# Kernel tuning notes

Hardware: AMD Instinct MI355X
Metric: run time of the kernel (lower is better)

## Reference

```python
import jax, jax.numpy as jnp
import numpy as np
from jax import lax

TEMP = 0.05
MOMENTUM = 0.9
EPS = 1e-12


def _l2_normalize(x, axis=-1):
    n = jnp.sqrt(jnp.sum(x * x, axis=axis, keepdims=True))
    return x / jnp.maximum(n, EPS)


def _cross_entropy(logits, targets):
    # mean over batch of -log_softmax(logits)[target]
    logp = jax.nn.log_softmax(logits, axis=-1)
    return -jnp.mean(jnp.take_along_axis(logp, targets[:, None], axis=-1))


def _momentum_update(features, x, targets, m):
    # Sequential per-sample read-modify-write (faithful to the torch loop,
    # matters when targets contain duplicates). carry = memory bank.
    def step(f, xy):
        x_i, y_i = xy
        row = m * f[y_i] + (1.0 - m) * x_i
        row = row / jnp.linalg.norm(row)
        return f.at[y_i].set(row), None
    f, _ = lax.scan(step, features, (x, targets))
    return f


def setup_inputs() -> dict:
    key = jax.random.key(0)
    k1, k2, k3, k4, k5, k6 = jax.random.split(key, 6)
    B, D, N = 512, 1024, 16384
    inputs_rgb = jax.random.normal(k1, (B, D), dtype=jnp.float32)
    inputs_ir = jax.random.normal(k2, (B, D), dtype=jnp.float32)
    targets_rgb = jax.random.randint(k3, (B,), 0, N, dtype=jnp.int32)
    targets_ir = jax.random.randint(k4, (B,), 0, N, dtype=jnp.int32)
    # memory banks (buffers); initialized as normalized random rows to mimic a
    # warmed-up cluster memory (the module starts at zeros, degenerate for CE)
    features_rgb = _l2_normalize(jax.random.normal(k5, (N, D), dtype=jnp.float32))
    features_ir = _l2_normalize(jax.random.normal(k6, (N, D), dtype=jnp.float32))
    return {"inputs_rgb": inputs_rgb, "inputs_ir": inputs_ir,
            "targets_rgb": targets_rgb, "targets_ir": targets_ir,
            "features_rgb": features_rgb, "features_ir": features_ir}


def reference(inputs_rgb, inputs_ir, targets_rgb, targets_ir, features_rgb, features_ir):
    x_rgb = _l2_normalize(inputs_rgb)  # [B, D]
    x_ir = _l2_normalize(inputs_ir)
    logits_rgb = (x_rgb @ features_rgb.T) / TEMP  # [B, N]
    logits_ir = (x_ir @ features_ir.T) / TEMP
    loss_rgb = _cross_entropy(logits_rgb, targets_rgb)
    loss_ir = _cross_entropy(logits_ir, targets_ir)
    # side-effect of CM.backward in the original: momentum scatter update + renorm
    # (change_scale == 1.0 so the Hungarian cross-modal exchange is skipped)
    new_features_rgb = _momentum_update(features_rgb, x_rgb, targets_rgb, MOMENTUM)
    new_features_ir = _momentum_update(features_ir, x_ir, targets_ir, MOMENTUM)
    return (loss_rgb, loss_ir, new_features_rgb, new_features_ir)
```

## Files before the change

kernel.cpp:

```cpp
#include <hip/hip_runtime.h>
#include <math.h>

#define BATCH 512
#define DIM   1024
#define NCLUS 16384
#define TINV  20.0f

typedef __attribute__((ext_vector_type(4))) float f32x4;
typedef __attribute__((ext_vector_type(8))) short bf16x8;

static __device__ __forceinline__ unsigned short f2bf(float f) {
  unsigned int u = __float_as_uint(f);
  u += 0x7FFFu + ((u >> 16) & 1u);
  return (unsigned short)(u >> 16);
}

typedef const __attribute__((address_space(1))) unsigned int* gas1_t;
typedef __attribute__((address_space(3))) unsigned int* las3_t;
static __device__ __forceinline__ void gload16(const void* g, void* l) {
  __builtin_amdgcn_global_load_lds((gas1_t)g, (las3_t)l, 16, 0, 0);
}

__global__ void nrm_kernel(const float* __restrict__ in_rgb,
                           const float* __restrict__ in_ir,
                           float* __restrict__ xf,
                           unsigned short* __restrict__ xb,
                           float* __restrict__ accum) {
  int gid = blockIdx.x * blockDim.x + threadIdx.x;
  if (gid < 2048) accum[gid] = 0.0f;

  int row = blockIdx.x;
  int mod = row >> 9;
  int r   = row & 511;
  const float* in = (mod ? in_ir : in_rgb) + (size_t)r * DIM;
  float* xo          = xf + ((size_t)mod * BATCH + r) * DIM;
  unsigned short* xbo = xb + ((size_t)mod * BATCH + r) * DIM;

  int t = threadIdx.x;
  float4 v = ((const float4*)in)[t];
  float ss = v.x*v.x + v.y*v.y + v.z*v.z + v.w*v.w;
#pragma unroll
  for (int m = 1; m < 64; m <<= 1) ss += __shfl_xor(ss, m, 64);
  __shared__ float red[4];
  if ((t & 63) == 0) red[t >> 6] = ss;
  __syncthreads();
  float inv = 1.0f / fmaxf(sqrtf(red[0] + red[1] + red[2] + red[3]), 1e-12f);
  float4 o = make_float4(v.x * inv, v.y * inv, v.z * inv, v.w * inv);
  ((float4*)xo)[t] = o;
  ushort4 ob = make_ushort4(f2bf(o.x), f2bf(o.y), f2bf(o.z), f2bf(o.w));
  ((ushort4*)xbo)[t] = ob;
}

__global__ void cvtcopy_kernel(const float* __restrict__ f_rgb,
                               const float* __restrict__ f_ir,
                               float* __restrict__ out,
                               unsigned short* __restrict__ fb,
                               int precvt) {
  const size_t n4 = (size_t)NCLUS * DIM / 4;
  size_t stride = (size_t)gridDim.x * blockDim.x;
  for (size_t i = (size_t)blockIdx.x * blockDim.x + threadIdx.x; i < 2 * n4; i += stride) {
    const float4 v = (i < n4) ? ((const float4*)f_rgb)[i] : ((const float4*)f_ir)[i - n4];
    float2* o2 = (float2*)(out + 4 * i);
    o2[0] = make_float2(v.x, v.y);
    o2[1] = make_float2(v.z, v.w);
    if (precvt)
      ((ushort4*)fb)[i] = make_ushort4(f2bf(v.x), f2bf(v.y), f2bf(v.z), f2bf(v.w));
  }
}

#define BM 128
#define BN 128
#define BK 32

template<int PRECVT>
__global__ void gemm_lse_kernel(const unsigned short* __restrict__ xb,
                                const unsigned short* __restrict__ fb,
                                const float* __restrict__ f_rgb,
                                const float* __restrict__ f_ir,
                                const int* __restrict__ t_rgb,
                                const int* __restrict__ t_ir,
                                float* __restrict__ rowsum,
                                float* __restrict__ tgtlog) {
  const int nt  = blockIdx.x;
  const int bt  = blockIdx.y & 3;
  const int mod = blockIdx.y >> 2;

  const unsigned short* X  = xb + ((size_t)mod * BATCH + bt * BM) * DIM;
  const unsigned short* Bb = fb + ((size_t)mod * NCLUS + nt * BN) * DIM;
  const float* Ff = (mod ? f_ir : f_rgb) + (size_t)nt * BN * DIM;
  const int*   tg = mod ? t_ir : t_rgb;
  float* rs = rowsum + mod * BATCH;
  float* tl = tgtlog + mod * BATCH;

  __shared__ __align__(16) unsigned short As[2][BM * BK];
  __shared__ __align__(16) unsigned short Bs[2][BN * BK];

  const int tid  = threadIdx.x;
  const int wid  = tid >> 6;
  const int lane = tid & 63;
  const int wr = wid >> 1, wc = wid & 1;
  const int l15 = lane & 15, lhi = lane >> 4;

  f32x4 acc[4][4];
#pragma unroll
  for (int m = 0; m < 4; ++m)
#pragma unroll
    for (int n = 0; n < 4; ++n) acc[m][n] = (f32x4){0.f, 0.f, 0.f, 0.f};

  auto STAGE = [&](int buf, int kk) {
#pragma unroll
    for (int i = 0; i < 2; ++i) {
      int q = i * 256 + tid;
      gload16(X + (size_t)(q >> 2) * DIM + kk + (q & 3) * 8,
              &As[buf][(size_t)(i * 256 + wid * 64) * 8]);
      if (PRECVT)
        gload16(Bb + (size_t)(q >> 2) * DIM + kk + (q & 3) * 8,
                &Bs[buf][(size_t)(i * 256 + wid * 64) * 8]);
    }
    if (!PRECVT) {
#pragma unroll
      for (int i = 0; i < 4; ++i) {
        int id = i * 256 + tid;
        int row = id >> 3, c4 = (id & 7) << 2;
        float4 v = *(const float4*)(Ff + (size_t)row * DIM + kk + c4);
        *(ushort4*)(&Bs[buf][row * BK + c4]) =
            make_ushort4(f2bf(v.x), f2bf(v.y), f2bf(v.z), f2bf(v.w));
      }
    }
  };

  auto COMPUTE = [&](int buf) {
    bf16x8 a[4], b[4];
#pragma unroll
    for (int m = 0; m < 4; ++m)
      a[m] = *(const bf16x8*)(&As[buf][(wr * 64 + m * 16 + l15) * BK + lhi * 8]);
#pragma unroll
    for (int n = 0; n < 4; ++n)
      b[n] = *(const bf16x8*)(&Bs[buf][(wc * 64 + n * 16 + l15) * BK + lhi * 8]);
#pragma unroll
    for (int m = 0; m < 4; ++m)
#pragma unroll
      for (int n = 0; n < 4; ++n)
        acc[m][n] = __builtin_amdgcn_mfma_f32_16x16x32_bf16(a[m], b[n], acc[m][n], 0, 0, 0);
  };

  STAGE(0, 0);
  __syncthreads();
  int cur = 0;
  for (int s = 1; s < DIM / BK; ++s) {
    STAGE(cur ^ 1, s * BK);
    COMPUTE(cur);
    __syncthreads();
    cur ^= 1;
  }
  COMPUTE(cur);

#pragma unroll
  for (int m = 0; m < 4; ++m) {
    const int browbase = bt * BM + wr * 64 + m * 16 + lhi * 4;
    float esum[4];
#pragma unroll
    for (int j = 0; j < 4; ++j) {
      const int brow = browbase + j;
      const int t = tg[brow];
      float e = 0.f;
#pragma unroll
      for (int n = 0; n < 4; ++n) {
        float logit = acc[m][n][j] * TINV;
        e += __expf(logit);
        int col = nt * BN + wc * 64 + n * 16 + l15;
        if (col == t) tl[brow] = logit;
      }
      esum[j] = e;
    }
#pragma unroll
    for (int j = 0; j < 4; ++j) {
      float e = esum[j];
      e += __shfl_xor(e, 1, 64);
      e += __shfl_xor(e, 2, 64);
      e += __shfl_xor(e, 4, 64);
      e += __shfl_xor(e, 8, 64);
      if (l15 == 0) atomicAdd(rs + browbase + j, e);
    }
  }
}

__global__ void loss_kernel(const float* __restrict__ rowsum,
                            const float* __restrict__ tgtlog,
                            float* __restrict__ out) {
  int t = threadIdx.x;
  float lr = logf(rowsum[t]) - tgtlog[t];
  float li = logf(rowsum[BATCH + t]) - tgtlog[BATCH + t];
#pragma unroll
  for (int m = 1; m < 64; m <<= 1) { lr += __shfl_xor(lr, m, 64); li += __shfl_xor(li, m, 64); }
  __shared__ float sr[8], si[8];
  if ((t & 63) == 0) { sr[t >> 6] = lr; si[t >> 6] = li; }
  __syncthreads();
  if (t == 0) {
    float a = 0.f, b = 0.f;
#pragma unroll
    for (int i = 0; i < 8; ++i) { a += sr[i]; b += si[i]; }
    out[0] = a * (1.0f / BATCH);
    out[1] = b * (1.0f / BATCH);
  }
}

__global__ void mom_kernel(const int* __restrict__ t_rgb,
                           const int* __restrict__ t_ir,
                           const float* __restrict__ xf,
                           float* __restrict__ out) {
  const int i   = blockIdx.x;
  const int mod = blockIdx.y;
  const int* tg = mod ? t_ir : t_rgb;
  const int y = tg[i];
  for (int j = 0; j < i; ++j)
    if (tg[j] == y) return;

  const float* x = xf + (size_t)mod * BATCH * DIM;
  float* rowp = out + (size_t)mod * NCLUS * DIM + (size_t)y * DIM;

  const int t = threadIdx.x;
  float2 r0 = ((const float2*)rowp)[t];
  float2 r1 = ((const float2*)rowp)[t + 256];
  __shared__ float red[4];

  for (int j = i; j < BATCH; ++j) {
    if (tg[j] != y) continue;
    const float2* xr = (const float2*)(x + (size_t)j * DIM);
    float2 x0 = xr[t], x1 = xr[t + 256];
    r0.x = 0.9f * r0.x + 0.1f * x0.x;
    r0.y = 0.9f * r0.y + 0.1f * x0.y;
    r1.x = 0.9f * r1.x + 0.1f * x1.x;
    r1.y = 0.9f * r1.y + 0.1f * x1.y;
    float ss = r0.x*r0.x + r0.y*r0.y + r1.x*r1.x + r1.y*r1.y;
#pragma unroll
    for (int m = 1; m < 64; m <<= 1) ss += __shfl_xor(ss, m, 64);
    if ((t & 63) == 0) red[t >> 6] = ss;
    __syncthreads();
    float tot = red[0] + red[1] + red[2] + red[3];
    __syncthreads();
    float inv = 1.0f / sqrtf(tot);
    r0.x *= inv; r0.y *= inv; r1.x *= inv; r1.y *= inv;
  }
  ((float2*)rowp)[t] = r0;
  ((float2*)rowp)[t + 256] = r1;
}

extern "C" void kernel_launch(void* const* d_in, const int* in_sizes, int n_in,
                              void* d_out, int out_size, void* d_ws, size_t ws_size,
                              hipStream_t stream) {
  (void)in_sizes; (void)n_in; (void)out_size;
  const float* in_rgb = (const float*)d_in[0];
  const float* in_ir  = (const float*)d_in[1];
  const int*   t_rgb  = (const int*)d_in[2];
  const int*   t_ir   = (const int*)d_in[3];
  const float* f_rgb  = (const float*)d_in[4];
  const float* f_ir   = (const float*)d_in[5];
  float* out = (float*)d_out;

  char* ws = (char*)d_ws;
  float*          xf     = (float*)ws;
  unsigned short* xb     = (unsigned short*)(ws + (4u<<20));
  float*          rowsum = (float*)(ws + (6u<<20));
  float*          tgtlog = rowsum + 1024;
  unsigned short* fb     = (unsigned short*)(ws + (8u<<20));
  const int precvt = (ws_size >= ((size_t)72 << 20)) ? 1 : 0;

  nrm_kernel<<<1024, 256, 0, stream>>>(in_rgb, in_ir, xf, xb, rowsum);
  cvtcopy_kernel<<<2048, 256, 0, stream>>>(f_rgb, f_ir, out + 2, fb, precvt);
  if (precvt)
    gemm_lse_kernel<1><<<dim3(128, 8), 256, 0, stream>>>(xb, fb, f_rgb, f_ir,
                                                         t_rgb, t_ir, rowsum, tgtlog);
  else
    gemm_lse_kernel<0><<<dim3(128, 8), 256, 0, stream>>>(xb, fb, f_rgb, f_ir,
                                                         t_rgb, t_ir, rowsum, tgtlog);
  mom_kernel<<<dim3(512, 2), 256, 0, stream>>>(t_rgb, t_ir, xf, out + 2);
  loss_kernel<<<1, 512, 0, stream>>>(rowsum, tgtlog, out);
}
```

Before: 191.1 us.

## Fuse feature-bank copy and bf16 conversion into GEMM B-tile staging

Removes the separate cvtcopy kernel that copied both fp32 memory banks to the output and pre-converted them to bf16. The GEMM now loads fp32 B tiles into registers, converts them to bf16 into LDS, and has the bt==0 blocks write the fp32 copy to the output. Register prefetch of the next B tile is issued before the MFMA compute so the load latency overlaps with compute. This saves a full extra read and write of the 128MB banks, but each bank is now read four times in fp32 (once per batch tile) and register pressure goes up.

```diff
diff --git a/kernel.cpp b/kernel.cpp
--- a/kernel.cpp
+++ b/kernel.cpp
@@ -51,43 +51,26 @@
   ((ushort4*)xbo)[t] = ob;
 }
 
-__global__ void cvtcopy_kernel(const float* __restrict__ f_rgb,
-                               const float* __restrict__ f_ir,
-                               float* __restrict__ out,
-                               unsigned short* __restrict__ fb,
-                               int precvt) {
-  const size_t n4 = (size_t)NCLUS * DIM / 4;
-  size_t stride = (size_t)gridDim.x * blockDim.x;
-  for (size_t i = (size_t)blockIdx.x * blockDim.x + threadIdx.x; i < 2 * n4; i += stride) {
-    const float4 v = (i < n4) ? ((const float4*)f_rgb)[i] : ((const float4*)f_ir)[i - n4];
-    float2* o2 = (float2*)(out + 4 * i);
-    o2[0] = make_float2(v.x, v.y);
-    o2[1] = make_float2(v.z, v.w);
-    if (precvt)
-      ((ushort4*)fb)[i] = make_ushort4(f2bf(v.x), f2bf(v.y), f2bf(v.z), f2bf(v.w));
-  }
-}
-
 #define BM 128
 #define BN 128
 #define BK 32
-
-template<int PRECVT>
+#define NSTEP (DIM / BK)
+
 __global__ void gemm_lse_kernel(const unsigned short* __restrict__ xb,
-                                const unsigned short* __restrict__ fb,
                                 const float* __restrict__ f_rgb,
                                 const float* __restrict__ f_ir,
                                 const int* __restrict__ t_rgb,
                                 const int* __restrict__ t_ir,
+                                float* __restrict__ outc,
                                 float* __restrict__ rowsum,
                                 float* __restrict__ tgtlog) {
   const int nt  = blockIdx.x;
   const int bt  = blockIdx.y & 3;
   const int mod = blockIdx.y >> 2;
 
-  const unsigned short* X  = xb + ((size_t)mod * BATCH + bt * BM) * DIM;
-  const unsigned short* Bb = fb + ((size_t)mod * NCLUS + nt * BN) * DIM;
+  const unsigned short* X = xb + ((size_t)mod * BATCH + bt * BM) * DIM;
   const float* Ff = (mod ? f_ir : f_rgb) + (size_t)nt * BN * DIM;
+  float* Oc = outc + ((size_t)mod * NCLUS + (size_t)nt * BN) * DIM;
   const int*   tg = mod ? t_ir : t_rgb;
   float* rs = rowsum + mod * BATCH;
   float* tl = tgtlog + mod * BATCH;
@@ -107,25 +90,34 @@
 #pragma unroll
     for (int n = 0; n < 4; ++n) acc[m][n] = (f32x4){0.f, 0.f, 0.f, 0.f};
 
-  auto STAGE = [&](int buf, int kk) {
+  auto B_LOAD = [&](float4* br, int kk) {
+#pragma unroll
+    for (int i = 0; i < 4; ++i) {
+      int id = i * 256 + tid;
+      br[i] = *(const float4*)(Ff + (size_t)(id >> 3) * DIM + kk + ((id & 7) << 2));
+    }
+  };
+  auto B_WRITE = [&](int buf, const float4* br, int kk) {
+#pragma unroll
+    for (int i = 0; i < 4; ++i) {
+      int id = i * 256 + tid;
+      int row = id >> 3, c4 = (id & 7) << 2;
+      float4 v = br[i];
+      *(ushort4*)(&Bs[buf][row * BK + c4]) =
+          make_ushort4(f2bf(v.x), f2bf(v.y), f2bf(v.z), f2bf(v.w));
+      if (bt == 0) {
+        float2* o2 = (float2*)(Oc + (size_t)row * DIM + kk + c4);
+        o2[0] = make_float2(v.x, v.y);
+        o2[1] = make_float2(v.z, v.w);
+      }
+    }
+  };
+  auto A_STAGE = [&](int buf, int kk) {
 #pragma unroll
     for (int i = 0; i < 2; ++i) {
       int q = i * 256 + tid;
       gload16(X + (size_t)(q >> 2) * DIM + kk + (q & 3) * 8,
               &As[buf][(size_t)(i * 256 + wid * 64) * 8]);
-      if (PRECVT)
-        gload16(Bb + (size_t)(q >> 2) * DIM + kk + (q & 3) * 8,
-                &Bs[buf][(size_t)(i * 256 + wid * 64) * 8]);
-    }
-    if (!PRECVT) {
-#pragma unroll
-      for (int i = 0; i < 4; ++i) {
-        int id = i * 256 + tid;
-        int row = id >> 3, c4 = (id & 7) << 2;
-        float4 v = *(const float4*)(Ff + (size_t)row * DIM + kk + c4);
-        *(ushort4*)(&Bs[buf][row * BK + c4]) =
-            make_ushort4(f2bf(v.x), f2bf(v.y), f2bf(v.z), f2bf(v.w));
-      }
     }
   };
 
@@ -144,12 +136,20 @@
         acc[m][n] = __builtin_amdgcn_mfma_f32_16x16x32_bf16(a[m], b[n], acc[m][n], 0, 0, 0);
   };
 
-  STAGE(0, 0);
+  {
+    float4 br[4];
+    B_LOAD(br, 0);
+    A_STAGE(0, 0);
+    B_WRITE(0, br, 0);
+  }
   __syncthreads();
   int cur = 0;
-  for (int s = 1; s < DIM / BK; ++s) {
-    STAGE(cur ^ 1, s * BK);
+  for (int s = 1; s < NSTEP; ++s) {
+    float4 brn[4];
+    B_LOAD(brn, s * BK);
     COMPUTE(cur);
+    A_STAGE(cur ^ 1, s * BK);
+    B_WRITE(cur ^ 1, brn, s * BK);
     __syncthreads();
     cur ^= 1;
   }
@@ -249,7 +249,7 @@
 extern "C" void kernel_launch(void* const* d_in, const int* in_sizes, int n_in,
                               void* d_out, int out_size, void* d_ws, size_t ws_size,
                               hipStream_t stream) {
-  (void)in_sizes; (void)n_in; (void)out_size;
+  (void)in_sizes; (void)n_in; (void)out_size; (void)ws_size;
   const float* in_rgb = (const float*)d_in[0];
   const float* in_ir  = (const float*)d_in[1];
   const int*   t_rgb  = (const int*)d_in[2];
@@ -263,17 +263,10 @@
   unsigned short* xb     = (unsigned short*)(ws + (4u<<20));
   float*          rowsum = (float*)(ws + (6u<<20));
   float*          tgtlog = rowsum + 1024;
-  unsigned short* fb     = (unsigned short*)(ws + (8u<<20));
-  const int precvt = (ws_size >= ((size_t)72 << 20)) ? 1 : 0;
 
   nrm_kernel<<<1024, 256, 0, stream>>>(in_rgb, in_ir, xf, xb, rowsum);
-  cvtcopy_kernel<<<2048, 256, 0, stream>>>(f_rgb, f_ir, out + 2, fb, precvt);
-  if (precvt)
-    gemm_lse_kernel<1><<<dim3(128, 8), 256, 0, stream>>>(xb, fb, f_rgb, f_ir,
-                                                         t_rgb, t_ir, rowsum, tgtlog);
-  else
-    gemm_lse_kernel<0><<<dim3(128, 8), 256, 0, stream>>>(xb, fb, f_rgb, f_ir,
-                                                         t_rgb, t_ir, rowsum, tgtlog);
+  gemm_lse_kernel<<<dim3(128, 8), 256, 0, stream>>>(xb, f_rgb, f_ir, t_rgb, t_ir,
+                                                    out + 2, rowsum, tgtlog);
   mom_kernel<<<dim3(512, 2), 256, 0, stream>>>(t_rgb, t_ir, xf, out + 2);
   loss_kernel<<<1, 512, 0, stream>>>(rowsum, tgtlog, out);
 }
```

Result: slower. 195.5 us (+2.3%).
